# Kernel optimization log

Measured on AMD Instinct MI355X. Metric: run time of the kernel, lower is better.

The kernel has to match this reference:

```python
import jax, jax.numpy as jnp
import numpy as np

N = 100000          # instances in the bag
L_IN = 784          # 28*28
C = 128             # size[1]
H = 2               # n_heads = len(temperature)
S = C // H          # step = 64
D = S // 2          # per-head hidden dim ('small') = 32
TEMP = jnp.array([1.0, 1.0], dtype=jnp.float32)  # temperature per head


def setup_inputs() -> dict:
    key = jax.random.key(0)
    ks = jax.random.split(key, 8)
    h = jax.random.normal(ks[0], (N, L_IN), dtype=jnp.float32)
    # shared FC: Linear(784, 128) (xavier-normal-ish init, zero bias)
    W0 = jax.random.normal(ks[1], (L_IN, C), dtype=jnp.float32) * (2.0 / (L_IN + C)) ** 0.5
    b0 = jnp.zeros((C,), dtype=jnp.float32)
    # per-head gated attention nets, stacked over head axis
    Wa = jax.random.normal(ks[2], (H, S, D), dtype=jnp.float32) * (2.0 / (S + D)) ** 0.5
    ba = jnp.zeros((H, D), dtype=jnp.float32)
    Wb = jax.random.normal(ks[3], (H, S, D), dtype=jnp.float32) * (2.0 / (S + D)) ** 0.5
    bb = jnp.zeros((H, D), dtype=jnp.float32)
    Wc = jax.random.normal(ks[4], (H, D, 1), dtype=jnp.float32) * (2.0 / (D + 1)) ** 0.5
    bc = jnp.zeros((H, 1), dtype=jnp.float32)
    # bag-level classifier: Linear(128, 1)
    Wcls = jax.random.normal(ks[5], (C, 1), dtype=jnp.float32) * (2.0 / (C + 1)) ** 0.5
    bcls = jnp.zeros((1,), dtype=jnp.float32)
    return {"h": h, "W0": W0, "b0": b0, "Wa": Wa, "ba": ba,
            "Wb": Wb, "bb": bb, "Wc": Wc, "bc": bc,
            "Wcls": Wcls, "bcls": bcls}


def reference(h, W0, b0, Wa, ba, Wb, bb, Wc, bc, Wcls, bcls):
    # shared FC + ReLU: [N,784] -> [N,128]
    x = jax.nn.relu(h @ W0 + b0)
    x = x.reshape(-1, H, S)                                  # [N,H,S]
    # gated attention per head, batched over heads via einsum
    a = jnp.tanh(jnp.einsum('nhs,hsd->nhd', x, Wa) + ba)     # [N,H,D]
    g = jax.nn.sigmoid(jnp.einsum('nhs,hsd->nhd', x, Wb) + bb)
    A = (jnp.einsum('nhd,hdo->nho', a * g, Wc) + bc)[..., 0] # [N,H]
    A = A / TEMP                                             # temperature scaling per head
    Aw = jax.nn.softmax(A, axis=0)                           # softmax over instances N
    # weighted instance pooling: [1, H*S] = [1, 128]
    M = jnp.einsum('nh,nhs->hs', Aw, x).reshape(1, H * S)
    logits = (M @ Wcls + bcls)[:, 0]                         # [1]
    Y_prob = jax.nn.sigmoid(logits)
    Y_hat = (Y_prob >= 0.5).astype(jnp.float32)
    return (Y_prob, Y_hat)
```

## Files before the change

kernel.cpp:

```cpp
#include <hip/hip_runtime.h>
#include <stdint.h>
#include <math.h>

typedef unsigned short u16;
typedef unsigned int   u32;
typedef __bf16 bf16x8 __attribute__((ext_vector_type(8)));
typedef float  f32x4  __attribute__((ext_vector_type(4)));

#define L_IN 784
#define KPAD 832
#define KT_N 13

__device__ __forceinline__ u32 f2bf(float f){
    u32 u = __float_as_uint(f);
    return (u + 0x7fffu + ((u >> 16) & 1u)) >> 16;
}

__device__ __forceinline__ void gload16(const void* g, void* l){
    __builtin_amdgcn_global_load_lds(
        (const __attribute__((address_space(1))) unsigned char*)g,
        (__attribute__((address_space(3))) unsigned char*)l, 16, 0, 0);
}

__global__ void prep_all(const float* __restrict__ W0, const float* __restrict__ Wa,
                         const float* __restrict__ Wb, u16* __restrict__ Bimg,
                         u16* __restrict__ Wab){
    int idx = blockIdx.x * 256 + threadIdx.x;
    if (idx < KPAD * 128){
        int col = idx & 127, k = idx >> 7;
        float v = (k < L_IN) ? W0[idx] : 0.f;
        int kt = k >> 6, kk = (k >> 5) & 1, j = k & 7, sl = (k >> 3) & 3;
        Bimg[(((kt * 2 + kk) * 8 + (col >> 4)) << 9) + (sl * 16 + (col & 15)) * 8 + j]
            = (u16)f2bf(v);
    } else if (idx < KPAD * 128 + 16384){
        int i2 = idx - KPAD * 128;
        int jj = i2 & 7, l = (i2 >> 3) & 63, ks = (i2 >> 9) & 1;
        int nt = (i2 >> 10) & 1, h = (i2 >> 11) & 1, mat = (i2 >> 12) & 1;
        int s = ks * 32 + (l >> 4) * 8 + jj, d = nt * 16 + (l & 15);
        const float* W = mat ? Wb : Wa;
        Wab[i2] = (u16)f2bf(W[h * 2048 + s * 32 + d]);
    }
}

__global__ __launch_bounds__(256, 3)
void fc_fused(const float* __restrict__ hG, const u16* __restrict__ Bimg,
              const u16* __restrict__ Wab, const float* __restrict__ b0,
              const float* __restrict__ ba, const float* __restrict__ bb,
              const float* __restrict__ Wc, const float* __restrict__ bc,
              float* __restrict__ partials, int N){
    __shared__ __align__(16) char Asm[3 * 16384];

    const int t    = threadIdx.x;
    const int lane = t & 63;
    const int w    = t >> 6;
    const int lr   = lane & 15;
    const int lk   = lane >> 4;
    const int gb   = blockIdx.x;
    const long rowBase = (long)gb * 64;

    const int rloc = t >> 4;
    const int csw  = (t & 15) ^ ((rloc & 3) << 1);
    const float* srcp[4];
    #pragma unroll
    for (int j = 0; j < 4; ++j){
        long grow = rowBase + j * 16 + rloc;
        if (grow >= N) grow = N - 1;
        srcp[j] = hG + grow * L_IN + csw * 4;
    }

    f32x4 acc[8];
    #pragma unroll
    for (int nt = 0; nt < 8; ++nt) acc[nt] = (f32x4)0.f;

    auto stage = [&](int kt, char* regn){
        #pragma unroll
        for (int j = 0; j < 4; ++j){
            const float* src = (kt == KT_N - 1 && csw >= 4)
                             ? (srcp[j] - csw * 4)
                             : (srcp[j] + kt * 64);
            gload16(src, regn + (j * 256 + t) * 16);
        }
    };

    char* p0 = &Asm[0];
    char* p1 = &Asm[16384];
    char* p2 = &Asm[32768];
    stage(0, p0);
    stage(1, p1);

    const int rA = w * 16 + lr;

    #pragma unroll 1
    for (int kt = 0; kt < KT_N; ++kt){
        if (kt == 0) __syncthreads();
        else         __builtin_amdgcn_s_barrier();
        __builtin_amdgcn_sched_barrier(0);

        const u16* bp = Bimg + (size_t)(kt * 2) * 4096 + lane * 8;
        bf16x8 b0f[8], b1f[8];
        #pragma unroll
        for (int nt = 0; nt < 8; ++nt)
            b0f[nt] = *(const bf16x8*)(bp + nt * 512);
        #pragma unroll
        for (int nt = 0; nt < 8; ++nt)
            b1f[nt] = *(const bf16x8*)(bp + 4096 + nt * 512);
        __builtin_amdgcn_sched_barrier(0);

        if (kt + 2 < KT_N) stage(kt + 2, p2);
        __builtin_amdgcn_sched_barrier(0);

        #pragma unroll
        for (int kk = 0; kk < 2; ++kk){
            const int q = kk * 4 + (lk ^ (rA & 3));
            f32x4 lo = *(const f32x4*)(p0 + (rA * 64 + q * 8) * 4);
            f32x4 hi = *(const f32x4*)(p0 + (rA * 64 + q * 8 + 4) * 4);
            bf16x8 af;
            #pragma unroll
            for (int j = 0; j < 4; ++j){
                af[j]     = (__bf16)lo[j];
                af[4 + j] = (__bf16)hi[j];
            }
            #pragma unroll
            for (int nt = 0; nt < 8; ++nt)
                acc[nt] = __builtin_amdgcn_mfma_f32_16x16x32_bf16(
                              af, kk ? b1f[nt] : b0f[nt], acc[nt], 0, 0, 0);
        }
        char* tmp = p0; p0 = p1; p1 = p2; p2 = tmp;
    }

    __syncthreads();

    u16*   xs   = (u16*)&Asm[0];
    float* pbuf = (float*)&Asm[16384];
    #pragma unroll
    for (int nt = 0; nt < 8; ++nt){
        float bias = b0[nt * 16 + lr];
        #pragma unroll
        for (int j = 0; j < 4; ++j){
            float v = acc[nt][j] + bias;
            v = v > 0.f ? v : 0.f;
            acc[nt][j] = v;
            int row = w * 16 + lk * 4 + j;
            int col = nt * 16 + lr;
            xs[row * 128 + ((((col >> 3) ^ (row & 15))) << 3) + (col & 7)] = (u16)f2bf(v);
        }
    }
    __syncthreads();

    float eh[2][4];
    #pragma unroll
    for (int h = 0; h < 2; ++h){
        bf16x8 xa[2];
        #pragma unroll
        for (int ks = 0; ks < 2; ++ks){
            int row = w * 16 + lr;
            int ch  = (h * 8 + ks * 4 + lk) ^ (row & 15);
            xa[ks] = *(const bf16x8*)&xs[row * 128 + ch * 8];
        }
        f32x4 Ca[2], Cg[2];
        #pragma unroll
        for (int nt = 0; nt < 2; ++nt){ Ca[nt] = (f32x4)0.f; Cg[nt] = (f32x4)0.f; }
        #pragma unroll
        for (int nt = 0; nt < 2; ++nt)
            #pragma unroll
            for (int ks = 0; ks < 2; ++ks){
                bf16x8 wfa = *(const bf16x8*)(Wab + ((size_t)(h*4 + nt*2 + ks) << 9) + lane * 8);
                bf16x8 wfb = *(const bf16x8*)(Wab + ((size_t)(8 + h*4 + nt*2 + ks) << 9) + lane * 8);
                Ca[nt] = __builtin_amdgcn_mfma_f32_16x16x32_bf16(xa[ks], wfa, Ca[nt], 0, 0, 0);
                Cg[nt] = __builtin_amdgcn_mfma_f32_16x16x32_bf16(xa[ks], wfb, Cg[nt], 0, 0, 0);
            }
        float pj[4];
        #pragma unroll
        for (int j = 0; j < 4; ++j){
            float s = 0.f;
            #pragma unroll
            for (int nt = 0; nt < 2; ++nt){
                int d = h * 32 + nt * 16 + lr;
                float av = tanhf(Ca[nt][j] + ba[d]);
                float gv = 1.f / (1.f + expf(-(Cg[nt][j] + bb[d])));
                s += av * gv * Wc[d];
            }
            pj[j] = s;
        }
        #pragma unroll
        for (int m = 1; m <= 8; m <<= 1)
            #pragma unroll
            for (int j = 0; j < 4; ++j)
                pj[j] += __shfl_xor(pj[j], m, 64);
        #pragma unroll
        for (int j = 0; j < 4; ++j){
            long row = rowBase + w * 16 + lk * 4 + j;
            eh[h][j] = (row < (long)N) ? expf(pj[j] + bc[h]) : 0.f;
        }
    }

    float p[8];
    #pragma unroll
    for (int nt = 0; nt < 8; ++nt){
        const int h = nt >> 2;
        float s = 0.f;
        #pragma unroll
        for (int j = 0; j < 4; ++j) s += eh[h][j] * acc[nt][j];
        p[nt] = s;
    }
    #pragma unroll
    for (int m = 16; m <= 32; m <<= 1)
        #pragma unroll
        for (int nt = 0; nt < 8; ++nt)
            p[nt] += __shfl_xor(p[nt], m, 64);
    float es0 = eh[0][0] + eh[0][1] + eh[0][2] + eh[0][3];
    float es1 = eh[1][0] + eh[1][1] + eh[1][2] + eh[1][3];
    es0 += __shfl_xor(es0, 16, 64); es0 += __shfl_xor(es0, 32, 64);
    es1 += __shfl_xor(es1, 16, 64); es1 += __shfl_xor(es1, 32, 64);

    if (lk == 0){
        #pragma unroll
        for (int nt = 0; nt < 8; ++nt)
            pbuf[w * 132 + nt * 16 + lr] = p[nt];
    }
    if (lane == 0){
        pbuf[w * 132 + 128] = es0;
        pbuf[w * 132 + 129] = es1;
    }
    __syncthreads();
    if (t < 130){
        float s = pbuf[t] + pbuf[132 + t] + pbuf[264 + t] + pbuf[396 + t];
        partials[(size_t)gb * 132 + t] = s;
    }
}

__global__ __launch_bounds__(256)
void reduce1(const float* __restrict__ partials, float* __restrict__ red, int nb){
    const int b = blockIdx.x, t = threadIdx.x;
    if (t >= 130) return;
    float a0 = 0.f, a1 = 0.f;
    for (int r = b; r < nb; r += 256){
        a0 += partials[(size_t)r * 132 + t];
        if (r + 128 < nb) a1 += partials[(size_t)(r + 128) * 132 + t];
    }
    red[b * 132 + t] = a0 + a1;
}

__global__ __launch_bounds__(256)
void finalize2(const float* __restrict__ red, const float* __restrict__ Wcls,
               const float* __restrict__ bcls, float* __restrict__ out){
    __shared__ double colD[2][130];
    __shared__ float  M_s[128];
    const int t = threadIdx.x;
    const int c = t & 127, rh = t >> 7;
    {
        double s = 0.0;
        for (int r = rh * 64; r < rh * 64 + 64; r += 4){
            s += (double)red[(r + 0) * 132 + c] + (double)red[(r + 1) * 132 + c]
               + (double)red[(r + 2) * 132 + c] + (double)red[(r + 3) * 132 + c];
        }
        colD[rh][c] = s;
    }
    if (t < 4){
        int cc = 128 + (t & 1), hh = t >> 1;
        double s = 0.0;
        for (int r = hh * 64; r < hh * 64 + 64; r += 4){
            s += (double)red[(r + 0) * 132 + cc] + (double)red[(r + 1) * 132 + cc]
               + (double)red[(r + 2) * 132 + cc] + (double)red[(r + 3) * 132 + cc];
        }
        colD[hh][cc] = s;
    }
    __syncthreads();
    if (t < 128)
        M_s[t] = (float)((colD[0][t] + colD[1][t]) /
                         (colD[0][128 + (t >> 6)] + colD[1][128 + (t >> 6)]));
    __syncthreads();
    if (t < 64){
        double d = (double)M_s[t] * (double)Wcls[t]
                 + (double)M_s[t + 64] * (double)Wcls[t + 64];
        #pragma unroll
        for (int m = 1; m < 64; m <<= 1) d += __shfl_xor(d, m, 64);
        if (t == 0){
            double lg = d + (double)bcls[0];
            out[0] = (float)(1.0 / (1.0 + exp(-lg)));
            out[1] = (lg >= 0.0) ? 1.f : 0.f;
        }
    }
}

extern "C" void kernel_launch(void* const* d_in, const int* in_sizes, int n_in,
                              void* d_out, int out_size, void* d_ws, size_t ws_size,
                              hipStream_t stream){
    const float* hG   = (const float*)d_in[0];
    const float* W0   = (const float*)d_in[1];
    const float* b0   = (const float*)d_in[2];
    const float* Wa   = (const float*)d_in[3];
    const float* ba   = (const float*)d_in[4];
    const float* Wb   = (const float*)d_in[5];
    const float* bb   = (const float*)d_in[6];
    const float* Wc   = (const float*)d_in[7];
    const float* bc   = (const float*)d_in[8];
    const float* Wcls = (const float*)d_in[9];
    const float* bcls = (const float*)d_in[10];

    const int N    = in_sizes[0] / L_IN;
    const int nb64 = (N + 63) / 64;

    char* ws = (char*)d_ws;
    u16* Bimg = (u16*)ws;
    u16* Wab  = (u16*)(ws + 262144);
    size_t poff = 262144 + 16384;
    float* partials = (float*)(ws + poff);
    size_t roff = poff + (((size_t)nb64 * 132 * 4 + 4095) & ~(size_t)4095);
    float* red  = (float*)(ws + roff);

    prep_all <<<(KPAD * 128 + 16384 + 255) / 256, 256, 0, stream>>>(W0, Wa, Wb, Bimg, Wab);
    fc_fused <<<nb64, 256, 0, stream>>>(hG, Bimg, Wab, b0, ba, bb, Wc, bc,
                                        partials, N);
    reduce1  <<<128, 256, 0, stream>>>(partials, red, nb64);
    finalize2<<<1, 256, 0, stream>>>(red, Wcls, bcls, (float*)d_out);
}
```

Baseline: 115.3 us.

## Use 128-row blocks with 32-wide K steps to reuse B fragments across two M tiles

New measurement: 124.7 us. +8.1%, slower.

```diff
diff --git a/kernel.cpp b/kernel.cpp
--- a/kernel.cpp
+++ b/kernel.cpp
@@ -8,8 +8,7 @@
 typedef float  f32x4  __attribute__((ext_vector_type(4)));
 
 #define L_IN 784
-#define KPAD 832
-#define KT_N 13
+#define KT2 25
 
 __device__ __forceinline__ u32 f2bf(float f){
     u32 u = __float_as_uint(f);
@@ -26,14 +25,14 @@
                          const float* __restrict__ Wb, u16* __restrict__ Bimg,
                          u16* __restrict__ Wab){
     int idx = blockIdx.x * 256 + threadIdx.x;
-    if (idx < KPAD * 128){
+    if (idx < KT2 * 32 * 128){
         int col = idx & 127, k = idx >> 7;
         float v = (k < L_IN) ? W0[idx] : 0.f;
-        int kt = k >> 6, kk = (k >> 5) & 1, j = k & 7, sl = (k >> 3) & 3;
-        Bimg[(((kt * 2 + kk) * 8 + (col >> 4)) << 9) + (sl * 16 + (col & 15)) * 8 + j]
+        int kt2 = k >> 5, lk = (k >> 3) & 3, j = k & 7;
+        Bimg[((kt2 * 8 + (col >> 4)) << 9) + (lk * 16 + (col & 15)) * 8 + j]
             = (u16)f2bf(v);
-    } else if (idx < KPAD * 128 + 16384){
-        int i2 = idx - KPAD * 128;
+    } else if (idx < KT2 * 32 * 128 + 16384){
+        int i2 = idx - KT2 * 32 * 128;
         int jj = i2 & 7, l = (i2 >> 3) & 63, ks = (i2 >> 9) & 1;
         int nt = (i2 >> 10) & 1, h = (i2 >> 11) & 1, mat = (i2 >> 12) & 1;
         int s = ks * 32 + (l >> 4) * 8 + jj, d = nt * 16 + (l & 15);
@@ -56,30 +55,28 @@
     const int lr   = lane & 15;
     const int lk   = lane >> 4;
     const int gb   = blockIdx.x;
-    const long rowBase = (long)gb * 64;
-
-    const int rloc = t >> 4;
-    const int csw  = (t & 15) ^ ((rloc & 3) << 1);
+    const long rowBase = (long)gb * 128;
+
+    const int cs = (t & 7) ^ ((t >> 3) & 7);
     const float* srcp[4];
     #pragma unroll
     for (int j = 0; j < 4; ++j){
-        long grow = rowBase + j * 16 + rloc;
+        long grow = rowBase + j * 32 + (t >> 3);
         if (grow >= N) grow = N - 1;
-        srcp[j] = hG + grow * L_IN + csw * 4;
-    }
-
-    f32x4 acc[8];
-    #pragma unroll
-    for (int nt = 0; nt < 8; ++nt) acc[nt] = (f32x4)0.f;
-
-    auto stage = [&](int kt, char* regn){
-        #pragma unroll
-        for (int j = 0; j < 4; ++j){
-            const float* src = (kt == KT_N - 1 && csw >= 4)
-                             ? (srcp[j] - csw * 4)
-                             : (srcp[j] + kt * 64);
-            gload16(src, regn + (j * 256 + t) * 16);
-        }
+        srcp[j] = hG + grow * L_IN + cs * 4;
+    }
+
+    f32x4 acc[2][8];
+    #pragma unroll
+    for (int mt = 0; mt < 2; ++mt)
+        #pragma unroll
+        for (int nt = 0; nt < 8; ++nt) acc[mt][nt] = (f32x4)0.f;
+
+    auto stage = [&](int kt, char* buf){
+        const int off = (kt == KT2 - 1 && cs >= 4) ? 0 : kt * 32;
+        #pragma unroll
+        for (int j = 0; j < 4; ++j)
+            gload16(srcp[j] + off, buf + (j * 256 + t) * 16);
     };
 
     char* p0 = &Asm[0];
@@ -88,32 +85,28 @@
     stage(0, p0);
     stage(1, p1);
 
-    const int rA = w * 16 + lr;
-
     #pragma unroll 1
-    for (int kt = 0; kt < KT_N; ++kt){
+    for (int kt = 0; kt < KT2; ++kt){
         if (kt == 0) __syncthreads();
         else         __builtin_amdgcn_s_barrier();
         __builtin_amdgcn_sched_barrier(0);
 
-        const u16* bp = Bimg + (size_t)(kt * 2) * 4096 + lane * 8;
-        bf16x8 b0f[8], b1f[8];
+        const u16* bp = Bimg + (size_t)kt * 4096 + lane * 8;
+        bf16x8 bfr[8];
         #pragma unroll
         for (int nt = 0; nt < 8; ++nt)
-            b0f[nt] = *(const bf16x8*)(bp + nt * 512);
-        #pragma unroll
-        for (int nt = 0; nt < 8; ++nt)
-            b1f[nt] = *(const bf16x8*)(bp + 4096 + nt * 512);
+            bfr[nt] = *(const bf16x8*)(bp + nt * 512);
         __builtin_amdgcn_sched_barrier(0);
 
-        if (kt + 2 < KT_N) stage(kt + 2, p2);
+        if (kt + 2 < KT2) stage(kt + 2, p2);
         __builtin_amdgcn_sched_barrier(0);
 
         #pragma unroll
-        for (int kk = 0; kk < 2; ++kk){
-            const int q = kk * 4 + (lk ^ (rA & 3));
-            f32x4 lo = *(const f32x4*)(p0 + (rA * 64 + q * 8) * 4);
-            f32x4 hi = *(const f32x4*)(p0 + (rA * 64 + q * 8 + 4) * 4);
+        for (int mt = 0; mt < 2; ++mt){
+            const int rA = w * 32 + mt * 16 + lr;
+            const char* base = p0 + rA * 128;
+            f32x4 lo = *(const f32x4*)(base + (((lk * 2)    ) ^ (rA & 7)) * 16);
+            f32x4 hi = *(const f32x4*)(base + (((lk * 2) + 1) ^ (rA & 7)) * 16);
             bf16x8 af;
             #pragma unroll
             for (int j = 0; j < 4; ++j){
@@ -122,8 +115,8 @@
             }
             #pragma unroll
             for (int nt = 0; nt < 8; ++nt)
-                acc[nt] = __builtin_amdgcn_mfma_f32_16x16x32_bf16(
-                              af, kk ? b1f[nt] : b0f[nt], acc[nt], 0, 0, 0);
+                acc[mt][nt] = __builtin_amdgcn_mfma_f32_16x16x32_bf16(
+                                  af, bfr[nt], acc[mt][nt], 0, 0, 0);
         }
         char* tmp = p0; p0 = p1; p1 = p2; p2 = tmp;
     }
@@ -131,68 +124,72 @@
     __syncthreads();
 
     u16*   xs   = (u16*)&Asm[0];
-    float* pbuf = (float*)&Asm[16384];
-    #pragma unroll
-    for (int nt = 0; nt < 8; ++nt){
-        float bias = b0[nt * 16 + lr];
-        #pragma unroll
-        for (int j = 0; j < 4; ++j){
-            float v = acc[nt][j] + bias;
-            v = v > 0.f ? v : 0.f;
-            acc[nt][j] = v;
-            int row = w * 16 + lk * 4 + j;
-            int col = nt * 16 + lr;
-            xs[row * 128 + ((((col >> 3) ^ (row & 15))) << 3) + (col & 7)] = (u16)f2bf(v);
-        }
-    }
-    __syncthreads();
-
-    float eh[2][4];
-    #pragma unroll
-    for (int h = 0; h < 2; ++h){
-        bf16x8 xa[2];
-        #pragma unroll
-        for (int ks = 0; ks < 2; ++ks){
-            int row = w * 16 + lr;
-            int ch  = (h * 8 + ks * 4 + lk) ^ (row & 15);
-            xa[ks] = *(const bf16x8*)&xs[row * 128 + ch * 8];
-        }
-        f32x4 Ca[2], Cg[2];
-        #pragma unroll
-        for (int nt = 0; nt < 2; ++nt){ Ca[nt] = (f32x4)0.f; Cg[nt] = (f32x4)0.f; }
-        #pragma unroll
-        for (int nt = 0; nt < 2; ++nt)
+    float* pbuf = (float*)&Asm[32768];
+    #pragma unroll
+    for (int mt = 0; mt < 2; ++mt)
+        #pragma unroll
+        for (int nt = 0; nt < 8; ++nt){
+            float bias = b0[nt * 16 + lr];
+            #pragma unroll
+            for (int j = 0; j < 4; ++j){
+                float v = acc[mt][nt][j] + bias;
+                v = v > 0.f ? v : 0.f;
+                acc[mt][nt][j] = v;
+                int row = w * 32 + mt * 16 + lk * 4 + j;
+                int col = nt * 16 + lr;
+                xs[row * 128 + (((col >> 3) ^ (row & 15)) << 3) + (col & 7)] = (u16)f2bf(v);
+            }
+        }
+    __syncthreads();
+
+    float eh[2][2][4];
+    #pragma unroll
+    for (int mt = 0; mt < 2; ++mt)
+        #pragma unroll
+        for (int h = 0; h < 2; ++h){
+            const int row = w * 32 + mt * 16 + lr;
+            bf16x8 xa[2];
             #pragma unroll
             for (int ks = 0; ks < 2; ++ks){
-                bf16x8 wfa = *(const bf16x8*)(Wab + ((size_t)(h*4 + nt*2 + ks) << 9) + lane * 8);
-                bf16x8 wfb = *(const bf16x8*)(Wab + ((size_t)(8 + h*4 + nt*2 + ks) << 9) + lane * 8);
-                Ca[nt] = __builtin_amdgcn_mfma_f32_16x16x32_bf16(xa[ks], wfa, Ca[nt], 0, 0, 0);
-                Cg[nt] = __builtin_amdgcn_mfma_f32_16x16x32_bf16(xa[ks], wfb, Cg[nt], 0, 0, 0);
-            }
-        float pj[4];
-        #pragma unroll
-        for (int j = 0; j < 4; ++j){
-            float s = 0.f;
-            #pragma unroll
-            for (int nt = 0; nt < 2; ++nt){
-                int d = h * 32 + nt * 16 + lr;
-                float av = tanhf(Ca[nt][j] + ba[d]);
-                float gv = 1.f / (1.f + expf(-(Cg[nt][j] + bb[d])));
-                s += av * gv * Wc[d];
-            }
-            pj[j] = s;
-        }
-        #pragma unroll
-        for (int m = 1; m <= 8; m <<= 1)
-            #pragma unroll
-            for (int j = 0; j < 4; ++j)
-                pj[j] += __shfl_xor(pj[j], m, 64);
-        #pragma unroll
-        for (int j = 0; j < 4; ++j){
-            long row = rowBase + w * 16 + lk * 4 + j;
-            eh[h][j] = (row < (long)N) ? expf(pj[j] + bc[h]) : 0.f;
-        }
-    }
+                int ch = (h * 8 + ks * 4 + lk) ^ (row & 15);
+                xa[ks] = *(const bf16x8*)&xs[row * 128 + ch * 8];
+            }
+            f32x4 Ca[2], Cg[2];
+            #pragma unroll
+            for (int nt = 0; nt < 2; ++nt){ Ca[nt] = (f32x4)0.f; Cg[nt] = (f32x4)0.f; }
+            #pragma unroll
+            for (int nt = 0; nt < 2; ++nt)
+                #pragma unroll
+                for (int ks = 0; ks < 2; ++ks){
+                    bf16x8 wfa = *(const bf16x8*)(Wab + ((size_t)(h*4 + nt*2 + ks) << 9) + lane * 8);
+                    bf16x8 wfb = *(const bf16x8*)(Wab + ((size_t)(8 + h*4 + nt*2 + ks) << 9) + lane * 8);
+                    Ca[nt] = __builtin_amdgcn_mfma_f32_16x16x32_bf16(xa[ks], wfa, Ca[nt], 0, 0, 0);
+                    Cg[nt] = __builtin_amdgcn_mfma_f32_16x16x32_bf16(xa[ks], wfb, Cg[nt], 0, 0, 0);
+                }
+            float pj[4];
+            #pragma unroll
+            for (int j = 0; j < 4; ++j){
+                float s = 0.f;
+                #pragma unroll
+                for (int nt = 0; nt < 2; ++nt){
+                    int d = h * 32 + nt * 16 + lr;
+                    float av = tanhf(Ca[nt][j] + ba[d]);
+                    float gv = 1.f / (1.f + expf(-(Cg[nt][j] + bb[d])));
+                    s += av * gv * Wc[d];
+                }
+                pj[j] = s;
+            }
+            #pragma unroll
+            for (int m = 1; m <= 8; m <<= 1)
+                #pragma unroll
+                for (int j = 0; j < 4; ++j)
+                    pj[j] += __shfl_xor(pj[j], m, 64);
+            #pragma unroll
+            for (int j = 0; j < 4; ++j){
+                long grow = rowBase + w * 32 + mt * 16 + lk * 4 + j;
+                eh[mt][h][j] = (grow < (long)N) ? expf(pj[j] + bc[h]) : 0.f;
+            }
+        }
 
     float p[8];
     #pragma unroll
@@ -200,7 +197,9 @@
         const int h = nt >> 2;
         float s = 0.f;
         #pragma unroll
-        for (int j = 0; j < 4; ++j) s += eh[h][j] * acc[nt][j];
+        for (int mt = 0; mt < 2; ++mt)
+            #pragma unroll
+            for (int j = 0; j < 4; ++j) s += eh[mt][h][j] * acc[mt][nt][j];
         p[nt] = s;
     }
     #pragma unroll
@@ -208,8 +207,11 @@
         #pragma unroll
         for (int nt = 0; nt < 8; ++nt)
             p[nt] += __shfl_xor(p[nt], m, 64);
-    float es0 = eh[0][0] + eh[0][1] + eh[0][2] + eh[0][3];
-    float es1 = eh[1][0] + eh[1][1] + eh[1][2] + eh[1][3];
+    float es0 = 0.f, es1 = 0.f;
+    #pragma unroll
+    for (int mt = 0; mt < 2; ++mt)
+        #pragma unroll
+        for (int j = 0; j < 4; ++j){ es0 += eh[mt][0][j]; es1 += eh[mt][1][j]; }
     es0 += __shfl_xor(es0, 16, 64); es0 += __shfl_xor(es0, 32, 64);
     es1 += __shfl_xor(es1, 16, 64); es1 += __shfl_xor(es1, 32, 64);
 
@@ -298,20 +300,20 @@
     const float* Wcls = (const float*)d_in[9];
     const float* bcls = (const float*)d_in[10];
 
-    const int N    = in_sizes[0] / L_IN;
-    const int nb64 = (N + 63) / 64;
+    const int N     = in_sizes[0] / L_IN;
+    const int nb128 = (N + 127) / 128;
 
     char* ws = (char*)d_ws;
     u16* Bimg = (u16*)ws;
     u16* Wab  = (u16*)(ws + 262144);
     size_t poff = 262144 + 16384;
     float* partials = (float*)(ws + poff);
-    size_t roff = poff + (((size_t)nb64 * 132 * 4 + 4095) & ~(size_t)4095);
+    size_t roff = poff + (((size_t)nb128 * 132 * 4 + 4095) & ~(size_t)4095);
     float* red  = (float*)(ws + roff);
 
-    prep_all <<<(KPAD * 128 + 16384 + 255) / 256, 256, 0, stream>>>(W0, Wa, Wb, Bimg, Wab);
-    fc_fused <<<nb64, 256, 0, stream>>>(hG, Bimg, Wab, b0, ba, bb, Wc, bc,
-                                        partials, N);
-    reduce1  <<<128, 256, 0, stream>>>(partials, red, nb64);
+    prep_all <<<(KT2 * 32 * 128 + 16384 + 255) / 256, 256, 0, stream>>>(W0, Wa, Wb, Bimg, Wab);
+    fc_fused <<<nb128, 256, 0, stream>>>(hG, Bimg, Wab, b0, ba, bb, Wc, bc,
+                                         partials, N);
+    reduce1  <<<128, 256, 0, stream>>>(partials, red, nb128);
     finalize2<<<1, 256, 0, stream>>>(red, Wcls, bcls, (float*)d_out);
 }
```

## Stage W0 tiles through LDS with async loads and finer K-steps

Applied to the files above, without the earlier changes.

Result: faster. 100.8 us (-12.6%).

```diff
diff --git a/kernel.cpp b/kernel.cpp
--- a/kernel.cpp
+++ b/kernel.cpp
@@ -8,8 +8,7 @@
 typedef float  f32x4  __attribute__((ext_vector_type(4)));
 
 #define L_IN 784
-#define KPAD 832
-#define KT_N 13
+#define KT2 25
 
 __device__ __forceinline__ u32 f2bf(float f){
     u32 u = __float_as_uint(f);
@@ -26,14 +25,14 @@
                          const float* __restrict__ Wb, u16* __restrict__ Bimg,
                          u16* __restrict__ Wab){
     int idx = blockIdx.x * 256 + threadIdx.x;
-    if (idx < KPAD * 128){
+    if (idx < KT2 * 32 * 128){
         int col = idx & 127, k = idx >> 7;
         float v = (k < L_IN) ? W0[idx] : 0.f;
-        int kt = k >> 6, kk = (k >> 5) & 1, j = k & 7, sl = (k >> 3) & 3;
-        Bimg[(((kt * 2 + kk) * 8 + (col >> 4)) << 9) + (sl * 16 + (col & 15)) * 8 + j]
+        int kt = k >> 5, lk = (k >> 3) & 3, j = k & 7;
+        Bimg[((kt * 8 + (col >> 4)) << 9) + (lk * 16 + (col & 15)) * 8 + j]
             = (u16)f2bf(v);
-    } else if (idx < KPAD * 128 + 16384){
-        int i2 = idx - KPAD * 128;
+    } else if (idx < KT2 * 32 * 128 + 16384){
+        int i2 = idx - KT2 * 32 * 128;
         int jj = i2 & 7, l = (i2 >> 3) & 63, ks = (i2 >> 9) & 1;
         int nt = (i2 >> 10) & 1, h = (i2 >> 11) & 1, mat = (i2 >> 12) & 1;
         int s = ks * 32 + (l >> 4) * 8 + jj, d = nt * 16 + (l & 15);
@@ -48,7 +47,7 @@
               const float* __restrict__ ba, const float* __restrict__ bb,
               const float* __restrict__ Wc, const float* __restrict__ bc,
               float* __restrict__ partials, int N){
-    __shared__ __align__(16) char Asm[3 * 16384];
+    __shared__ __align__(16) char Asm[6 * 8192];
 
     const int t    = threadIdx.x;
     const int lane = t & 63;
@@ -58,80 +57,80 @@
     const int gb   = blockIdx.x;
     const long rowBase = (long)gb * 64;
 
-    const int rloc = t >> 4;
-    const int csw  = (t & 15) ^ ((rloc & 3) << 1);
-    const float* srcp[4];
-    #pragma unroll
-    for (int j = 0; j < 4; ++j){
-        long grow = rowBase + j * 16 + rloc;
+    const int cs = (t & 7) ^ ((t >> 3) & 7);
+    const float* srcp[2];
+    #pragma unroll
+    for (int j = 0; j < 2; ++j){
+        long grow = rowBase + j * 32 + (t >> 3);
         if (grow >= N) grow = N - 1;
-        srcp[j] = hG + grow * L_IN + csw * 4;
-    }
+        srcp[j] = hG + grow * L_IN + cs * 4;
+    }
+    const char* BimgB = (const char*)Bimg;
 
     f32x4 acc[8];
     #pragma unroll
     for (int nt = 0; nt < 8; ++nt) acc[nt] = (f32x4)0.f;
 
-    auto stage = [&](int kt, char* regn){
+    auto stageA = [&](int kt, char* buf){
+        const int off = (kt == KT2 - 1 && cs >= 4) ? 0 : kt * 32;
+        #pragma unroll
+        for (int j = 0; j < 2; ++j)
+            gload16(srcp[j] + off, buf + (j * 256 + t) * 16);
+    };
+    auto stageB = [&](int kt, char* buf){
+        #pragma unroll
+        for (int i = 0; i < 2; ++i)
+            gload16(BimgB + (size_t)kt * 8192 + i * 4096 + t * 16,
+                    buf + i * 4096 + t * 16);
+    };
+
+    char* pa0 = &Asm[0];     char* pa1 = &Asm[8192];  char* pa2 = &Asm[16384];
+    char* pb0 = &Asm[24576]; char* pb1 = &Asm[32768]; char* pb2 = &Asm[40960];
+
+    stageA(0, pa0); stageB(0, pb0);
+    stageA(1, pa1); stageB(1, pb1);
+    __syncthreads();
+
+    const int rA = w * 16 + lr;
+
+    #pragma unroll 1
+    for (int kt = 0; kt < KT2; ++kt){
+        __builtin_amdgcn_sched_barrier(0);
+        if (kt + 2 < KT2){ stageA(kt + 2, pa2); stageB(kt + 2, pb2); }
+        __builtin_amdgcn_sched_barrier(0);
+
+        const char* base = pa0 + rA * 128;
+        f32x4 lo = *(const f32x4*)(base + (((lk * 2)    ) ^ (rA & 7)) * 16);
+        f32x4 hi = *(const f32x4*)(base + (((lk * 2) + 1) ^ (rA & 7)) * 16);
+        bf16x8 af;
         #pragma unroll
         for (int j = 0; j < 4; ++j){
-            const float* src = (kt == KT_N - 1 && csw >= 4)
-                             ? (srcp[j] - csw * 4)
-                             : (srcp[j] + kt * 64);
-            gload16(src, regn + (j * 256 + t) * 16);
-        }
-    };
-
-    char* p0 = &Asm[0];
-    char* p1 = &Asm[16384];
-    char* p2 = &Asm[32768];
-    stage(0, p0);
-    stage(1, p1);
-
-    const int rA = w * 16 + lr;
-
-    #pragma unroll 1
-    for (int kt = 0; kt < KT_N; ++kt){
-        if (kt == 0) __syncthreads();
-        else         __builtin_amdgcn_s_barrier();
-        __builtin_amdgcn_sched_barrier(0);
-
-        const u16* bp = Bimg + (size_t)(kt * 2) * 4096 + lane * 8;
-        bf16x8 b0f[8], b1f[8];
+            af[j]     = (__bf16)lo[j];
+            af[4 + j] = (__bf16)hi[j];
+        }
+        bf16x8 bfr[8];
         #pragma unroll
         for (int nt = 0; nt < 8; ++nt)
-            b0f[nt] = *(const bf16x8*)(bp + nt * 512);
+            bfr[nt] = *(const bf16x8*)(pb0 + nt * 1024 + lane * 16);
         #pragma unroll
         for (int nt = 0; nt < 8; ++nt)
-            b1f[nt] = *(const bf16x8*)(bp + 4096 + nt * 512);
-        __builtin_amdgcn_sched_barrier(0);
-
-        if (kt + 2 < KT_N) stage(kt + 2, p2);
-        __builtin_amdgcn_sched_barrier(0);
-
-        #pragma unroll
-        for (int kk = 0; kk < 2; ++kk){
-            const int q = kk * 4 + (lk ^ (rA & 3));
-            f32x4 lo = *(const f32x4*)(p0 + (rA * 64 + q * 8) * 4);
-            f32x4 hi = *(const f32x4*)(p0 + (rA * 64 + q * 8 + 4) * 4);
-            bf16x8 af;
-            #pragma unroll
-            for (int j = 0; j < 4; ++j){
-                af[j]     = (__bf16)lo[j];
-                af[4 + j] = (__bf16)hi[j];
-            }
-            #pragma unroll
-            for (int nt = 0; nt < 8; ++nt)
-                acc[nt] = __builtin_amdgcn_mfma_f32_16x16x32_bf16(
-                              af, kk ? b1f[nt] : b0f[nt], acc[nt], 0, 0, 0);
-        }
-        char* tmp = p0; p0 = p1; p1 = p2; p2 = tmp;
+            acc[nt] = __builtin_amdgcn_mfma_f32_16x16x32_bf16(af, bfr[nt], acc[nt], 0, 0, 0);
+
+        if (kt + 1 < KT2){
+            if (kt + 2 < KT2) asm volatile("s_waitcnt vmcnt(4)" ::: "memory");
+            else              asm volatile("s_waitcnt vmcnt(0)" ::: "memory");
+            __builtin_amdgcn_sched_barrier(0);
+            __builtin_amdgcn_s_barrier();
+            __builtin_amdgcn_sched_barrier(0);
+        }
+        char* ta = pa0; pa0 = pa1; pa1 = pa2; pa2 = ta;
+        char* tb = pb0; pb0 = pb1; pb1 = pb2; pb2 = tb;
     }
 
     __syncthreads();
 
     u16*   xs   = (u16*)&Asm[0];
-    float* pbuf = (float*)&Asm[16384];
+    float* pbuf = (float*)&Asm[24576];
     #pragma unroll
     for (int nt = 0; nt < 8; ++nt){
         float bias = b0[nt * 16 + lr];
@@ -309,7 +308,7 @@
     size_t roff = poff + (((size_t)nb64 * 132 * 4 + 4095) & ~(size_t)4095);
     float* red  = (float*)(ws + roff);
 
-    prep_all <<<(KPAD * 128 + 16384 + 255) / 256, 256, 0, stream>>>(W0, Wa, Wb, Bimg, Wab);
+    prep_all <<<(KT2 * 32 * 128 + 16384 + 255) / 256, 256, 0, stream>>>(W0, Wa, Wb, Bimg, Wab);
     fc_fused <<<nb64, 256, 0, stream>>>(hG, Bimg, Wab, b0, ba, bb, Wc, bc,
                                         partials, N);
     reduce1  <<<128, 256, 0, stream>>>(partials, red, nb64);
```
